# Kernel optimization log

Measured on AMD Instinct MI355X. Metric: run time of the kernel, lower is better.

The kernel has to match this reference:

```python
import jax, jax.numpy as jnp
import numpy as np
from functools import partial

EPS = 1e-3  # keras LayerNormalization default epsilon

def _conv_same(inp, w):
    # inp: [B,H,W,Cin], w: [k,k,Cin,Cout]
    return jax.lax.conv_general_dilated(
        inp, w, window_strides=(1, 1), padding='SAME',
        dimension_numbers=('NHWC', 'HWIO', 'NHWC'))

def _hard_sigmoid(x):
    # keras recurrent_activation default for ConvLSTM2D
    return jnp.clip(0.2 * x + 0.5, 0.0, 1.0)

def setup_inputs() -> dict:
    key = jax.random.key(0)
    k1, k2, k3 = jax.random.split(key, 3)
    B, T, H, W, C, F, K = 4, 16, 64, 64, 32, 64, 3
    x = jax.random.normal(k1, (B, T, H, W, C), dtype=jnp.float32)
    gamma = jnp.ones((C,), jnp.float32)
    beta = jnp.zeros((C,), jnp.float32)
    # gate order i, f, c, o stacked along output channels (keras convention)
    Wx = jax.random.normal(k2, (K, K, C, 4 * F), dtype=jnp.float32) * 0.05
    Wh = jax.random.normal(k3, (K, K, F, 4 * F), dtype=jnp.float32) * 0.05
    b = jnp.zeros((4 * F,), jnp.float32)
    return {"x": x, "gamma": gamma, "beta": beta, "Wx": Wx, "Wh": Wh, "b": b}

def reference(x, gamma, beta, Wx, Wh, b):
    B, T, H, W, C = x.shape
    F = Wh.shape[2]
    # LayerNorm over channel axis
    mu = jnp.mean(x, axis=-1, keepdims=True)
    var = jnp.var(x, axis=-1, keepdims=True)
    xn = (x - mu) * jax.lax.rsqrt(var + EPS) * gamma + beta

    # Precompute input-to-gate convs for all timesteps at once (time folded into batch)
    zx = _conv_same(xn.reshape(B * T, H, W, C), Wx) + b  # [B*T,H,W,4F]
    zx = zx.reshape(B, T, H, W, 4 * F).transpose(1, 0, 2, 3, 4)  # [T,B,H,W,4F]

    def step(carry, zxt):
        h, c = carry
        z = zxt + _conv_same(h, Wh)
        zi, zf, zc, zo = jnp.split(z, 4, axis=-1)
        i = _hard_sigmoid(zi)
        f = _hard_sigmoid(zf)
        c = f * c + i * jnp.tanh(zc)
        o = _hard_sigmoid(zo)
        h = o * jnp.tanh(c)
        return (h, c), h

    h0 = jnp.zeros((B, H, W, F), x.dtype)
    c0 = jnp.zeros((B, H, W, F), x.dtype)
    _, hs = jax.lax.scan(step, (h0, c0), zx)  # hs: [T,B,H,W,F]
    y = hs.transpose(1, 0, 2, 3, 4)  # [B,T,H,W,F] (return_sequences=True)

    # MaxPool3D pool_size=(1,2,2), stride = pool_size, VALID padding
    y = jax.lax.reduce_window(
        y, -jnp.inf, jax.lax.max,
        window_dimensions=(1, 1, 2, 2, 1),
        window_strides=(1, 1, 2, 2, 1),
        padding='VALID')
    return y
```

## Files before the change

kernel.cpp:

```cpp
#include <hip/hip_runtime.h>
#include <hip/hip_fp16.h>

typedef _Float16 f16;
typedef _Float16 f16x8 __attribute__((ext_vector_type(8)));
typedef float f32x4 __attribute__((ext_vector_type(4)));
typedef unsigned long long ull;

#define BB 4
#define TT 16
#define HH 64
#define WW 64
#define CC 32
#define FF 64
#define GG 256

#define WAITV(n) do { asm volatile("s_waitcnt vmcnt(" #n ")" ::: "memory"); \
                      __builtin_amdgcn_sched_barrier(0); } while (0)
#define LGKBAR do { asm volatile("s_waitcnt lgkmcnt(0)" ::: "memory"); \
                    __builtin_amdgcn_s_barrier(); \
                    __builtin_amdgcn_sched_barrier(0); } while (0)

__device__ __forceinline__ float hsig(float z) {
    return fminf(fmaxf(0.2f * z + 0.5f, 0.f), 1.f);
}
__device__ __forceinline__ float tanh_fast(float x) {
    return 1.f - 2.f / (__expf(2.f * x) + 1.f);
}

__device__ __forceinline__ void async_copy16(const void* g, void* l) {
    __builtin_amdgcn_global_load_lds(
        (const __attribute__((address_space(1))) unsigned*)g,
        (__attribute__((address_space(3))) unsigned*)l, 16, 0, 0);
}

__global__ void wprep_kernel(const float* __restrict__ wx, const float* __restrict__ wh,
                             f16* __restrict__ wcat) {
    int e = blockIdx.x * 256 + threadIdx.x;
    if (e < 9 * CC * GG) {
        int n = e & 255, k = e >> 8;
        int p = k / 96, r = k % 96;
        wcat[((p * 12 + (r >> 3)) * 256 + n) * 8 + (r & 7)] = (f16)wx[e];
    } else {
        e -= 9 * CC * GG;
        if (e < 9 * FF * GG) {
            int n = e & 255, k = 288 + (e >> 8);
            int p = k / 96, r = k % 96;
            wcat[((p * 12 + (r >> 3)) * 256 + n) * 8 + (r & 7)] = (f16)wh[e];
        }
    }
}

__device__ __forceinline__ void stage_x(const float* __restrict__ x, int bb, int t,
                                        int ty, int tx, int tid,
                                        const float* sg, const float* sb,
                                        f16* __restrict__ xpatch) {
    if (tid < 200) {
        int pix = tid >> 1, part = tid & 1;
        int py = pix / 10, px_ = pix % 10;
        int gy = ty * 8 - 1 + py, gx = tx * 8 - 1 + px_;
        if (gy >= 0 && gy < HH && gx >= 0 && gx < WW) {
            const float* xp = x + ((size_t)(bb * TT + t) * (HH * WW)
                                   + gy * WW + gx) * CC + part * 16;
            float v[16];
            float s = 0.f, s2 = 0.f;
#pragma unroll
            for (int j = 0; j < 4; j++) {
                float4 t4 = *(const float4*)(xp + j * 4);
                v[j * 4] = t4.x; v[j * 4 + 1] = t4.y; v[j * 4 + 2] = t4.z; v[j * 4 + 3] = t4.w;
                s += t4.x + t4.y + t4.z + t4.w;
                s2 += t4.x * t4.x + t4.y * t4.y + t4.z * t4.z + t4.w * t4.w;
            }
            s += __shfl_xor(s, 1);
            s2 += __shfl_xor(s2, 1);
            float mu = s * (1.f / CC);
            float var = s2 * (1.f / CC) - mu * mu;
            float rs = rsqrtf(var + 1e-3f);
            f16 o16[16];
#pragma unroll
            for (int c = 0; c < 16; c++)
                o16[c] = (f16)((v[c] - mu) * rs * sg[part * 16 + c] + sb[part * 16 + c]);
            f16x8* d = (f16x8*)&xpatch[pix * 72 + part * 16];
            d[0] = *(f16x8*)&o16[0];
            d[1] = *(f16x8*)&o16[8];
        }
    }
}

__global__ __launch_bounds__(512, 2)
void fused_kernel(const float* __restrict__ x, const float* __restrict__ gamma,
                  const float* __restrict__ beta, const f16* __restrict__ wcat,
                  const float* __restrict__ bs, f16* __restrict__ halo,
                  float* __restrict__ out, unsigned* __restrict__ flags) {
    __shared__ __align__(16) f16 patches[3 * 7200];
    __shared__ __align__(16) f16 wbuf[6 * 8192];
    __shared__ float sg[CC], sb[CC];

    f16* xpatch = patches;
    int tid = threadIdx.x;
    int tile = blockIdx.x;
    int bb = tile >> 6, ty = (tile >> 3) & 7, tx = tile & 7;
    int lane = tid & 63, w = tid >> 6;
    int wm = w >> 2, nhalf = (w >> 1) & 1, wn = w & 1;
    int quad = lane >> 4, noff = lane & 15;

    if (tid < CC) sg[tid] = gamma[tid];
    else if (tid < 2 * CC) sb[tid - CC] = beta[tid - CC];

    for (int i = tid; i < 2700; i += 512)
        ((f16x8*)patches)[i] = (f16x8){0, 0, 0, 0, 0, 0, 0, 0};

    const char* gwb = (const char*)wcat + w * 2048 + lane * 16;

    int fch = (nhalf << 5) + (wn << 4) + noff;
    float b_i = bs[fch], b_f = bs[64 + fch], b_c = bs[128 + fch], b_o = bs[192 + fch];

    float creg[2][4];
#pragma unroll
    for (int mt = 0; mt < 2; mt++)
#pragma unroll
        for (int r = 0; r < 4; r++) creg[mt][r] = 0.f;

    int mrow[2];
#pragma unroll
    for (int mt = 0; mt < 2; mt++) {
        int m = (wm << 5) + (mt << 4) + noff;
        mrow[mt] = ((m >> 3) * 10 + (m & 7)) * 72 + (quad << 3);
    }
    int rB[4];
#pragma unroll
    for (int cls = 0; cls < 4; cls++) rB[cls] = ((cls << 6) + fch) << 3;

    __syncthreads();

    stage_x(x, bb, 0, ty, tx, tid, sg, sb, xpatch);
#pragma unroll
    for (int k = 0; k < 3; k++) {
        async_copy16(gwb + (size_t)k * 16384, &wbuf[k * 8192 + w * 1024]);
        async_copy16(gwb + (size_t)k * 16384 + 1024, &wbuf[k * 8192 + w * 1024 + 512]);
    }

    for (int t = 0; t < TT; t++) {
        f16* hp_cur = patches + 7200 + (t & 1) * 7200;
        f16* hp_nxt = patches + 7200 + ((t + 1) & 1) * 7200;

        LGKBAR;

        f32x4 acc[2][4];
#pragma unroll
        for (int i = 0; i < 2; i++)
#pragma unroll
            for (int j = 0; j < 4; j++) acc[i][j] = (f32x4){0.f, 0.f, 0.f, 0.f};

#pragma unroll
        for (int g = 0; g < 9; ++g) {
            if (g > 0) LGKBAR;
            if (g == 2 && t > 0 && tid >= 256 && tid < 400) {
                int e = tid - 256;
                int hx = e >> 2, quarter = e & 3;
                int py, px_;
                if (hx < 10)      { py = 0; px_ = hx; }
                else if (hx < 20) { py = 9; px_ = hx - 10; }
                else if (hx < 28) { py = 1 + (hx - 20); px_ = 0; }
                else              { py = 1 + (hx - 28); px_ = 9; }
                int gy = ty * 8 - 1 + py, gx = tx * 8 - 1 + px_;
                if (gy >= 0 && gy < HH && gx >= 0 && gx < WW) {
                    int nb = bb * 64 + ((gy >> 3) << 3) + (gx >> 3);
                    while (__hip_atomic_load(&flags[nb], __ATOMIC_RELAXED,
                                             __HIP_MEMORY_SCOPE_AGENT) < (unsigned)t)
                        __builtin_amdgcn_s_sleep(1);
                    const ull* src = (const ull*)(halo + ((size_t)(t * BB + bb) * (HH * WW)
                                                         + gy * WW + gx) * FF) + quarter * 4;
                    f16* dst = &hp_cur[(py * 10 + px_) * 72 + quarter * 16];
#pragma unroll
                    for (int j = 0; j < 4; j++) {
                        ull vv = __hip_atomic_load(src + j, __ATOMIC_RELAXED,
                                                   __HIP_MEMORY_SCOPE_AGENT);
                        *(ull*)(dst + j * 4) = vv;
                    }
                }
            }
            if (g < 8) {
#pragma unroll
                for (int k = 0; k < 3; k++) {
                    int c = 3 * g + 3 + k;
                    async_copy16(gwb + (size_t)c * 16384,
                                 &wbuf[(c % 6) * 8192 + w * 1024]);
                    async_copy16(gwb + (size_t)c * 16384 + 1024,
                                 &wbuf[(c % 6) * 8192 + w * 1024 + 512]);
                }
            }
#pragma unroll
            for (int cw = 0; cw < 3; ++cw) {
                int c = g * 3 + cw;
                if (g < 8) { if (cw == 0) WAITV(10); else if (cw == 1) WAITV(8); else WAITV(6); }
                else       { if (cw == 0) WAITV(4);  else if (cw == 1) WAITV(2); else WAITV(0); }
                bool isx = c < 9;
                int hc = c - 9;
                int tap = isx ? c : (hc >> 1);
                int coff = isx ? 0 : ((hc & 1) << 5);
                const f16* ap = isx ? xpatch : hp_cur;
                int dy = tap / 3, dx = tap % 3;
                int toff = (dy * 10 + dx) * 72 + coff;
                f16x8 a[2];
#pragma unroll
                for (int mt = 0; mt < 2; mt++)
                    a[mt] = *(const f16x8*)&ap[mrow[mt] + toff];
                const f16* wbc = &wbuf[(c % 6) * 8192 + quad * 2048];
#pragma unroll
                for (int cls = 0; cls < 4; cls++) {
                    f16x8 bf = *(const f16x8*)&wbc[rB[cls]];
                    acc[0][cls] = __builtin_amdgcn_mfma_f32_16x16x32_f16(a[0], bf, acc[0][cls], 0, 0, 0);
                    acc[1][cls] = __builtin_amdgcn_mfma_f32_16x16x32_f16(a[1], bf, acc[1][cls], 0, 0, 0);
                }
            }
        }

#pragma unroll
        for (int mt = 0; mt < 2; mt++) {
#pragma unroll
            for (int r = 0; r < 4; r++) {
                int m = (wm << 5) + (mt << 4) + (quad << 2) + r;
                int py8 = m >> 3, px8 = m & 7;
                float zi = acc[mt][0][r] + b_i;
                float zf = acc[mt][1][r] + b_f;
                float zc = acc[mt][2][r] + b_c;
                float zo = acc[mt][3][r] + b_o;
                float ig = hsig(zi), fg = hsig(zf), og = hsig(zo);
                float cn = fg * creg[mt][r] + ig * tanh_fast(zc);
                creg[mt][r] = cn;
                f16 hval = (f16)(og * tanh_fast(cn));
                hp_nxt[((py8 + 1) * 10 + px8 + 1) * 72 + fch] = hval;
                if (py8 == 0 || py8 == 7 || px8 == 0 || px8 == 7) {
                    union { f16 f; unsigned short u; } cvt; cvt.f = hval;
                    unsigned short* hp = (unsigned short*)halo
                        + ((size_t)((t + 1) * BB + bb) * (HH * WW)
                           + (ty * 8 + py8) * WW + (tx * 8 + px8)) * FF + fch;
                    __hip_atomic_store(hp, cvt.u, __ATOMIC_RELAXED, __HIP_MEMORY_SCOPE_AGENT);
                }
            }
        }
        __syncthreads();
        if (tid == 0)
            __hip_atomic_store(&flags[tile], (unsigned)(t + 1), __ATOMIC_RELAXED,
                               __HIP_MEMORY_SCOPE_AGENT);

        {
            int o = tid * 2;
            int f0 = o & 63;
            int ox2 = (o >> 6) & 3, oy2 = (o >> 8) & 3;
            int row = 1 + oy2 * 2, col = 1 + ox2 * 2;
            const f16* hb = &hp_nxt[(row * 10 + col) * 72 + f0];
            float v0 = fmaxf(fmaxf((float)hb[0], (float)hb[72]),
                             fmaxf((float)hb[720], (float)hb[792]));
            float v1 = fmaxf(fmaxf((float)hb[1], (float)hb[73]),
                             fmaxf((float)hb[721], (float)hb[793]));
            size_t ofs = (((size_t)(bb * TT + t) * 32 + (ty * 4 + oy2)) * 32
                          + (tx * 4 + ox2)) * 64 + f0;
            float2 v2; v2.x = v0; v2.y = v1;
            *(float2*)(out + ofs) = v2;
        }

        if (t + 1 < TT) {
            stage_x(x, bb, t + 1, ty, tx, tid, sg, sb, xpatch);
#pragma unroll
            for (int k = 0; k < 3; k++) {
                async_copy16(gwb + (size_t)k * 16384, &wbuf[k * 8192 + w * 1024]);
                async_copy16(gwb + (size_t)k * 16384 + 1024, &wbuf[k * 8192 + w * 1024 + 512]);
            }
        }
    }
}

extern "C" void kernel_launch(void* const* d_in, const int* in_sizes, int n_in,
                              void* d_out, int out_size, void* d_ws, size_t ws_size,
                              hipStream_t stream) {
    const float* x = (const float*)d_in[0];
    const float* gamma = (const float*)d_in[1];
    const float* beta = (const float*)d_in[2];
    const float* wx = (const float*)d_in[3];
    const float* wh = (const float*)d_in[4];
    const float* bs = (const float*)d_in[5];
    float* out = (float*)d_out;

    char* ws = (char*)d_ws;
    f16* wcat = (f16*)(ws + 16777216);
    unsigned* flags = (unsigned*)(ws + 17219584);
    f16* hs = (f16*)(ws + 21413888);

    hipMemsetAsync(flags, 0, 256 * 4, stream);
    wprep_kernel<<<864, 256, 0, stream>>>(wx, wh, wcat);

    fused_kernel<<<256, 512, 0, stream>>>(x, gamma, beta, wcat, bs, hs, out, flags);
}
```

Baseline: 243.1 us.

## Software-pipeline LDS fragment reads against MFMAs and simplify weight-load waits

Restructures the inner gate-conv loop so the LDS fragments for the next chunk are read into a double-buffered register set while the MFMAs for the current chunk run, with MFMA sections raised in wave priority. The fine-grained per-chunk vmcnt waits are replaced by a full wait at the end of each group, and the next step's weight prefetch is issued before staging x, followed by a full wait. The aim is to hide LDS latency behind matrix math. The cost is more register pressure, and the coarser waits may expose global-load latency that the staggered waits used to overlap.

```diff
diff --git a/kernel.cpp b/kernel.cpp
--- a/kernel.cpp
+++ b/kernel.cpp
@@ -14,8 +14,7 @@
 #define FF 64
 #define GG 256
 
-#define WAITV(n) do { asm volatile("s_waitcnt vmcnt(" #n ")" ::: "memory"); \
-                      __builtin_amdgcn_sched_barrier(0); } while (0)
+#define WAITV(n) asm volatile("s_waitcnt vmcnt(" #n ")" ::: "memory")
 #define LGKBAR do { asm volatile("s_waitcnt lgkmcnt(0)" ::: "memory"); \
                     __builtin_amdgcn_s_barrier(); \
                     __builtin_amdgcn_sched_barrier(0); } while (0)
@@ -138,6 +137,7 @@
         async_copy16(gwb + (size_t)k * 16384, &wbuf[k * 8192 + w * 1024]);
         async_copy16(gwb + (size_t)k * 16384 + 1024, &wbuf[k * 8192 + w * 1024 + 512]);
     }
+    WAITV(0);
 
     for (int t = 0; t < TT; t++) {
         f16* hp_cur = patches + 7200 + (t & 1) * 7200;
@@ -151,9 +151,37 @@
 #pragma unroll
             for (int j = 0; j < 4; j++) acc[i][j] = (f32x4){0.f, 0.f, 0.f, 0.f};
 
+        f16x8 fA[2][2], fB[2][4];
+
+        auto READF = [&](int cn) {
+            const int pn = cn & 1;
+            const bool isx = cn < 9;
+            const int hc = cn - 9;
+            const int tap = isx ? cn : (hc >> 1);
+            const int coff = isx ? 0 : ((hc & 1) << 5);
+            const f16* ap = isx ? xpatch : hp_cur;
+            const int toff = ((tap / 3) * 10 + (tap % 3)) * 72 + coff;
+            fA[pn][0] = *(const f16x8*)&ap[mrow[0] + toff];
+            fA[pn][1] = *(const f16x8*)&ap[mrow[1] + toff];
+            const f16* wbc = &wbuf[(cn % 6) * 8192 + quad * 2048];
+#pragma unroll
+            for (int cls = 0; cls < 4; cls++)
+                fB[pn][cls] = *(const f16x8*)&wbc[rB[cls]];
+        };
+        auto MFMA8 = [&](int pc) {
+            __builtin_amdgcn_s_setprio(1);
+#pragma unroll
+            for (int cls = 0; cls < 4; cls++) {
+                acc[0][cls] = __builtin_amdgcn_mfma_f32_16x16x32_f16(fA[pc][0], fB[pc][cls], acc[0][cls], 0, 0, 0);
+                acc[1][cls] = __builtin_amdgcn_mfma_f32_16x16x32_f16(fA[pc][1], fB[pc][cls], acc[1][cls], 0, 0, 0);
+            }
+            __builtin_amdgcn_s_setprio(0);
+        };
+
 #pragma unroll
         for (int g = 0; g < 9; ++g) {
             if (g > 0) LGKBAR;
+            READF(3 * g);
             if (g == 2 && t > 0 && tid >= 256 && tid < 400) {
                 int e = tid - 256;
                 int hx = e >> 2, quarter = e & 3;
@@ -191,28 +219,11 @@
             }
 #pragma unroll
             for (int cw = 0; cw < 3; ++cw) {
-                int c = g * 3 + cw;
-                if (g < 8) { if (cw == 0) WAITV(10); else if (cw == 1) WAITV(8); else WAITV(6); }
-                else       { if (cw == 0) WAITV(4);  else if (cw == 1) WAITV(2); else WAITV(0); }
-                bool isx = c < 9;
-                int hc = c - 9;
-                int tap = isx ? c : (hc >> 1);
-                int coff = isx ? 0 : ((hc & 1) << 5);
-                const f16* ap = isx ? xpatch : hp_cur;
-                int dy = tap / 3, dx = tap % 3;
-                int toff = (dy * 10 + dx) * 72 + coff;
-                f16x8 a[2];
-#pragma unroll
-                for (int mt = 0; mt < 2; mt++)
-                    a[mt] = *(const f16x8*)&ap[mrow[mt] + toff];
-                const f16* wbc = &wbuf[(c % 6) * 8192 + quad * 2048];
-#pragma unroll
-                for (int cls = 0; cls < 4; cls++) {
-                    f16x8 bf = *(const f16x8*)&wbc[rB[cls]];
-                    acc[0][cls] = __builtin_amdgcn_mfma_f32_16x16x32_f16(a[0], bf, acc[0][cls], 0, 0, 0);
-                    acc[1][cls] = __builtin_amdgcn_mfma_f32_16x16x32_f16(a[1], bf, acc[1][cls], 0, 0, 0);
-                }
-            }
+                const int c = 3 * g + cw;
+                if (cw < 2) READF(c + 1);
+                MFMA8(c & 1);
+            }
+            if (g < 8) WAITV(0);
         }
 
 #pragma unroll
@@ -261,12 +272,13 @@
         }
 
         if (t + 1 < TT) {
-            stage_x(x, bb, t + 1, ty, tx, tid, sg, sb, xpatch);
 #pragma unroll
             for (int k = 0; k < 3; k++) {
                 async_copy16(gwb + (size_t)k * 16384, &wbuf[k * 8192 + w * 1024]);
                 async_copy16(gwb + (size_t)k * 16384 + 1024, &wbuf[k * 8192 + w * 1024 + 512]);
             }
+            stage_x(x, bb, t + 1, ty, tx, tid, sg, sb, xpatch);
+            WAITV(0);
         }
     }
 }
```

Measured after the change: 258.7 us. 6.4% more time.
